# Kernel tuning notes

Measured on AMD Instinct MI355X. Metric: run time of the kernel, lower is better.

## Reference

```python
import jax, jax.numpy as jnp
import numpy as np

# Static config (matches init_kwargs / spatial layout)
SHAPES = ((64, 64), (32, 32), (16, 16))   # (H, W) per level, bev=256 at /4,/8,/16
B, HEADS, LEVELS, POINTS, C = 2, 8, 3, 4, 256
HD = C // HEADS
NV = sum(h * w for h, w in SHAPES)        # 5376
NQ = NV
TP = HEADS * LEVELS * POINTS              # 96


def setup_inputs() -> dict:
    key = jax.random.key(0)
    ks = jax.random.split(key, 10)
    s = 1.0 / np.sqrt(C)
    inp = {
        'query': jax.random.normal(ks[0], (B, NQ, C), dtype=jnp.float32),
        'reference_points': jax.random.uniform(ks[1], (B, NQ, 2), dtype=jnp.float32),
        'value': jax.random.normal(ks[2], (B, NV, C), dtype=jnp.float32),
        'Wv': jax.random.normal(ks[3], (C, C), dtype=jnp.float32) * s,
        'bv': jnp.zeros((C,), dtype=jnp.float32),
        # offset proj: small scale so sampling stays local-ish (orig init is 0)
        'Woff': jax.random.normal(ks[4], (TP * 2, C), dtype=jnp.float32) * (0.02 * s),
        'boff': jnp.zeros((TP * 2,), dtype=jnp.float32),
        'Wa': jax.random.normal(ks[5], (TP, C), dtype=jnp.float32) * s,
        'ba': jnp.zeros((TP,), dtype=jnp.float32),
        'Wo': jax.random.normal(ks[6], (C, C), dtype=jnp.float32) * s,
        'bo': jnp.zeros((C,), dtype=jnp.float32),
    }
    return inp


def _msda(query, reference_points, value, Wv, bv, Woff, boff, Wa, ba, Wo, bo):
    Bb, nq, _ = query.shape
    # value projection -> per-head values
    v = (value @ Wv.T + bv).reshape(Bb, NV, HEADS, HD)
    # sampling offsets: (B, NQ, HEADS, LEVELS, POINTS, 2)
    off = (query @ Woff.T + boff).reshape(Bb, nq, HEADS, LEVELS, POINTS, 2)
    # attention weights: softmax over LEVELS*POINTS jointly
    a = (query @ Wa.T + ba).reshape(Bb, nq, HEADS, LEVELS * POINTS)
    a = jax.nn.softmax(a, axis=-1).reshape(Bb, nq, HEADS, LEVELS, POINTS)
    # sampling locations in [0,1] (clamp matches torch .clamp(0,1))
    loc = jnp.clip(reference_points[:, :, None, None, None, :] + off, 0.0, 1.0)

    out = jnp.zeros((Bb, HEADS, nq, HD), dtype=query.dtype)
    start = 0
    for lvl, (H, W) in enumerate(SHAPES):
        n = H * W
        # (B, HEADS, H*W, HD) flattened level feature map per head
        vl = jnp.transpose(v[:, start:start + n].reshape(Bb, H, W, HEADS, HD),
                           (0, 3, 1, 2, 4)).reshape(Bb, HEADS, n, HD)
        loc_l = loc[:, :, :, lvl]                     # (B, NQ, HEADS, K, 2)
        # align_corners=False unnormalization: ((g+1)*size - 1)/2 with g=2*loc-1
        x = loc_l[..., 0] * W - 0.5
        y = loc_l[..., 1] * H - 0.5
        x0 = jnp.floor(x)
        y0 = jnp.floor(y)
        wx1 = x - x0
        wy1 = y - y0
        x0i = x0.astype(jnp.int32)
        y0i = y0.astype(jnp.int32)
        acc = jnp.zeros((Bb, HEADS, nq * POINTS, HD), dtype=query.dtype)
        for dy in (0, 1):
            for dx in (0, 1):
                ix = x0i + dx
                iy = y0i + dy
                wgt = (wx1 if dx else 1.0 - wx1) * (wy1 if dy else 1.0 - wy1)
                # zero padding outside the map (padding_mode='zeros')
                valid = (ix >= 0) & (ix < W) & (iy >= 0) & (iy < H)
                idx = jnp.clip(iy, 0, H - 1) * W + jnp.clip(ix, 0, W - 1)
                idx_t = jnp.transpose(idx, (0, 2, 1, 3)).reshape(Bb, HEADS, nq * POINTS)
                g = jnp.take_along_axis(vl, idx_t[..., None], axis=2)  # (B,H,NQ*K,HD)
                w_t = jnp.transpose(wgt * valid.astype(wgt.dtype),
                                    (0, 2, 1, 3)).reshape(Bb, HEADS, nq * POINTS, 1)
                acc = acc + g * w_t
        aw = jnp.transpose(a[:, :, :, lvl], (0, 2, 1, 3)).reshape(Bb, HEADS, nq * POINTS, 1)
        out = out + (acc * aw).reshape(Bb, HEADS, nq, POINTS, HD).sum(axis=3)
        start += n
    out = jnp.transpose(out, (0, 2, 1, 3)).reshape(Bb, nq, C)
    return out @ Wo.T + bo


def reference(query, reference_points, value, Wv, bv, Woff, boff, Wa, ba, Wo, bo):
    return _msda(query, reference_points, value, Wv, bv, Woff, boff, Wa, ba, Wo, bo)
```

## Files before the change

kernel.cpp:

```cpp
#include <hip/hip_runtime.h>
#include <hip/hip_bf16.h>
#include <cmath>

#define BATCH   2
#define NQ      5376
#define NV      5376
#define CDIM    256
#define HEADS   8
#define HD      32
#define LEVELS  3
#define POINTS  4
#define TP      96
#define MROWS   (BATCH*NQ)
#define NOFF    (TP*2)
#define NQA     (NOFF+TP)
#define NQAP    320

typedef __attribute__((ext_vector_type(8))) short bf16x8;
typedef __attribute__((ext_vector_type(4))) float f32x4;
typedef unsigned short u16;
typedef unsigned int   u32;

#define AS1 __attribute__((address_space(1)))
#define AS3 __attribute__((address_space(3)))

__device__ __forceinline__ void g2lds16(const void* g, void* l) {
    __builtin_amdgcn_global_load_lds((const AS1 void*)g, (AS3 void*)l, 16, 0, 0);
}

__device__ __forceinline__ u16 bf_of(float f) {
    union { __hip_bfloat16 h; u16 s; } u;
    u.h = __float2bfloat16(f);
    return u.s;
}
__device__ __forceinline__ float bf_back(u16 s) {
    return __uint_as_float((u32)s << 16);
}

__device__ __forceinline__ ushort4 cvt_hi(float4 v) {
    ushort4 h;
    h.x = bf_of(v.x); h.y = bf_of(v.y); h.z = bf_of(v.z); h.w = bf_of(v.w);
    return h;
}
__device__ __forceinline__ ushort4 cvt_lo(float4 v, ushort4 h) {
    ushort4 l;
    l.x = bf_of(v.x - bf_back(h.x));
    l.y = bf_of(v.y - bf_back(h.y));
    l.z = bf_of(v.z - bf_back(h.z));
    l.w = bf_of(v.w - bf_back(h.w));
    return l;
}

#define NVAL8  344064
#define NQRY8  344064
#define NWV8   8192
#define NWOFF8 6144
#define NWA8   3072
#define NWO8   8192
#define NPAD8  1024
#define PREP_BLOCKS 2792
__global__ __launch_bounds__(256) void prep_kernel(
    const float* __restrict__ value, const float* __restrict__ query,
    const float* __restrict__ Wv, const float* __restrict__ Woff,
    const float* __restrict__ Wa, const float* __restrict__ Wo,
    u16* __restrict__ val_hi, u16* __restrict__ val_lo,
    u16* __restrict__ q_hi, u16* __restrict__ wv_h,
    u16* __restrict__ wqa_h, u16* __restrict__ wo_h)
{
    int r = blockIdx.x * 256 + threadIdx.x;

    if (r < NVAL8) {
        const float4 a0 = *reinterpret_cast<const float4*>(value + (size_t)r * 8);
        const float4 a1 = *reinterpret_cast<const float4*>(value + (size_t)r * 8 + 4);
        const ushort4 h0 = cvt_hi(a0), h1 = cvt_hi(a1);
        *reinterpret_cast<ushort4*>(val_hi + (size_t)r * 8)     = h0;
        *reinterpret_cast<ushort4*>(val_hi + (size_t)r * 8 + 4) = h1;
        *reinterpret_cast<ushort4*>(val_lo + (size_t)r * 8)     = cvt_lo(a0, h0);
        *reinterpret_cast<ushort4*>(val_lo + (size_t)r * 8 + 4) = cvt_lo(a1, h1);
        return;
    }
    r -= NVAL8;
    if (r < NQRY8) {
        const float4 a0 = *reinterpret_cast<const float4*>(query + (size_t)r * 8);
        const float4 a1 = *reinterpret_cast<const float4*>(query + (size_t)r * 8 + 4);
        *reinterpret_cast<ushort4*>(q_hi + (size_t)r * 8)     = cvt_hi(a0);
        *reinterpret_cast<ushort4*>(q_hi + (size_t)r * 8 + 4) = cvt_hi(a1);
        return;
    }
    r -= NQRY8;
    if (r < NWV8) {
        const float4 a0 = *reinterpret_cast<const float4*>(Wv + (size_t)r * 8);
        const float4 a1 = *reinterpret_cast<const float4*>(Wv + (size_t)r * 8 + 4);
        *reinterpret_cast<ushort4*>(wv_h + (size_t)r * 8)     = cvt_hi(a0);
        *reinterpret_cast<ushort4*>(wv_h + (size_t)r * 8 + 4) = cvt_hi(a1);
        return;
    }
    r -= NWV8;
    if (r < NWOFF8) {
        const float4 a0 = *reinterpret_cast<const float4*>(Woff + (size_t)r * 8);
        const float4 a1 = *reinterpret_cast<const float4*>(Woff + (size_t)r * 8 + 4);
        *reinterpret_cast<ushort4*>(wqa_h + (size_t)r * 8)     = cvt_hi(a0);
        *reinterpret_cast<ushort4*>(wqa_h + (size_t)r * 8 + 4) = cvt_hi(a1);
        return;
    }
    r -= NWOFF8;
    if (r < NWA8) {
        const float4 a0 = *reinterpret_cast<const float4*>(Wa + (size_t)r * 8);
        const float4 a1 = *reinterpret_cast<const float4*>(Wa + (size_t)r * 8 + 4);
        u16* dst = wqa_h + (size_t)NOFF * CDIM;
        *reinterpret_cast<ushort4*>(dst + (size_t)r * 8)     = cvt_hi(a0);
        *reinterpret_cast<ushort4*>(dst + (size_t)r * 8 + 4) = cvt_hi(a1);
        return;
    }
    r -= NWA8;
    if (r < NWO8) {
        const float4 a0 = *reinterpret_cast<const float4*>(Wo + (size_t)r * 8);
        const float4 a1 = *reinterpret_cast<const float4*>(Wo + (size_t)r * 8 + 4);
        *reinterpret_cast<ushort4*>(wo_h + (size_t)r * 8)     = cvt_hi(a0);
        *reinterpret_cast<ushort4*>(wo_h + (size_t)r * 8 + 4) = cvt_hi(a1);
        return;
    }
    r -= NWO8;
    const ushort4 z = {0, 0, 0, 0};
    u16* dst = wqa_h + (size_t)NQA * CDIM;
    *reinterpret_cast<ushort4*>(dst + (size_t)r * 8)     = z;
    *reinterpret_cast<ushort4*>(dst + (size_t)r * 8 + 4) = z;
}

#define GBM 64
#define GBN 64
#define GBK 32

#define VBLOCKS (168 * 4)
#define K1_BLOCKS (VBLOCKS + 168 * 5)
#define K1_CPX (K1_BLOCKS / 8)

__global__ __launch_bounds__(256) void gemm_vqa_kernel(
    const u16* __restrict__ val_hi, const u16* __restrict__ val_lo,
    const u16* __restrict__ q_hi,
    const u16* __restrict__ wv_h, const u16* __restrict__ wqa_h,
    const float* __restrict__ bv, const float* __restrict__ boff,
    const float* __restrict__ ba,
    u16* __restrict__ vOut, u16* __restrict__ offOut, u16* __restrict__ aOut)
{
    __shared__ __align__(16) u16 sAh[2][GBM * GBK];
    __shared__ __align__(16) u16 sAl[2][GBM * GBK];
    __shared__ __align__(16) u16 sBh[2][GBM * GBK];

    const int bid0 = blockIdx.x;
    const int bid = (bid0 & 7) * K1_CPX + (bid0 >> 3);

    const bool vpath = bid < VBLOCKS;
    int m0, n0;
    if (vpath) { m0 = (bid >> 2) * GBM;          n0 = (bid & 3) * GBM; }
    else       { const int b2 = bid - VBLOCKS;
                 m0 = (b2 / 5) * GBM;            n0 = (b2 % 5) * GBM; }

    const int tid  = threadIdx.x;
    const int lane = tid & 63;
    const int wave = tid >> 6;
    const int wr   = wave & 1;
    const int wc   = wave >> 1;
    const int qm   = lane & 15;
    const int quad = lane >> 4;

    const int arow = (wave << 4) + (lane >> 2);
    const int ak   = (lane & 3) * 8;

    const u16* Asrc_h = (vpath ? val_hi : q_hi) + (size_t)(m0 + arow) * CDIM + ak;
    const u16* Asrc_l = val_lo + (size_t)(m0 + arow) * CDIM + ak;
    const u16* Bsrc   = (vpath ? wv_h : wqa_h) + (size_t)(n0 + arow) * CDIM + ak;

    f32x4 acc[2][2];
    #pragma unroll
    for (int i = 0; i < 2; ++i)
        #pragma unroll
        for (int j = 0; j < 2; ++j)
            acc[i][j] = (f32x4){0.f, 0.f, 0.f, 0.f};

    {
        g2lds16(Asrc_h, &sAh[0][wave * 512]);
        if (vpath) g2lds16(Asrc_l, &sAl[0][wave * 512]);
        g2lds16(Bsrc, &sBh[0][wave * 512]);
    }
    __syncthreads();

    int cur = 0;
    for (int k0 = 0; k0 < CDIM; k0 += GBK) {
        if (k0 + GBK < CDIM) {
            g2lds16(Asrc_h + k0 + GBK, &sAh[cur ^ 1][wave * 512]);
            if (vpath) g2lds16(Asrc_l + k0 + GBK, &sAl[cur ^ 1][wave * 512]);
            g2lds16(Bsrc + k0 + GBK, &sBh[cur ^ 1][wave * 512]);
        }

        bf16x8 fah[2], fal[2], fbh[2];
        #pragma unroll
        for (int x = 0; x < 2; ++x) {
            const int rm = wr * 32 + x * 16 + qm;
            const int rn = wc * 32 + x * 16 + qm;
            fah[x] = *reinterpret_cast<const bf16x8*>(&sAh[cur][rm * GBK + quad * 8]);
            fbh[x] = *reinterpret_cast<const bf16x8*>(&sBh[cur][rn * GBK + quad * 8]);
            if (vpath)
                fal[x] = *reinterpret_cast<const bf16x8*>(&sAl[cur][rm * GBK + quad * 8]);
        }
        #pragma unroll
        for (int mi = 0; mi < 2; ++mi)
            #pragma unroll
            for (int ni = 0; ni < 2; ++ni) {
                acc[mi][ni] = __builtin_amdgcn_mfma_f32_16x16x32_bf16(
                    fah[mi], fbh[ni], acc[mi][ni], 0, 0, 0);
                if (vpath)
                    acc[mi][ni] = __builtin_amdgcn_mfma_f32_16x16x32_bf16(
                        fal[mi], fbh[ni], acc[mi][ni], 0, 0, 0);
            }
        __syncthreads();
        cur ^= 1;
    }

    #pragma unroll
    for (int mi = 0; mi < 2; ++mi) {
        #pragma unroll
        for (int ni = 0; ni < 2; ++ni) {
            const int n = n0 + wc * 32 + ni * 16 + qm;
            if (vpath) {
                const float bn = bv[n];
                #pragma unroll
                for (int r = 0; r < 4; ++r) {
                    const int m = m0 + wr * 32 + mi * 16 + quad * 4 + r;
                    const float val = acc[mi][ni][r] + bn;
                    const int b = m / NV, rr = m - b * NV;
                    const int h = n >> 5, c = n & 31;
                    vOut[(((size_t)b * HEADS + h) * NV + rr) * HD + c] = bf_of(val);
                }
            } else {
                if (n >= NQA) continue;
                const float bn = (n < NOFF) ? boff[n] : ba[n - NOFF];
                #pragma unroll
                for (int r = 0; r < 4; ++r) {
                    const int m = m0 + wr * 32 + mi * 16 + quad * 4 + r;
                    const float val = acc[mi][ni][r] + bn;
                    if (n < NOFF)
                        offOut[(size_t)m * NOFF + n] = bf_of(val);
                    else
                        aOut[(size_t)m * TP + (n - NOFF)] = bf_of(val);
                }
            }
        }
    }
}

#define K3_BLOCKS ((MROWS / GBM) * 4)
#define K3_CPX (K3_BLOCKS / 8)

__global__ __launch_bounds__(256) void gemm_out_kernel(
    const u16* __restrict__ Ah, const u16* __restrict__ wo_h,
    const float* __restrict__ bias, float* __restrict__ Cout)
{
    __shared__ __align__(16) u16 sAh[2][GBM * GBK];
    __shared__ __align__(16) u16 sBh[2][GBM * GBK];

    const int bid0 = blockIdx.x;
    const int bid = (bid0 & 7) * K3_CPX + (bid0 >> 3);
    const int m0 = (bid >> 2) * GBM;
    const int n0 = (bid & 3) * GBM;

    const int tid  = threadIdx.x;
    const int lane = tid & 63;
    const int wave = tid >> 6;
    const int wr   = wave & 1;
    const int wc   = wave >> 1;
    const int qm   = lane & 15;
    const int quad = lane >> 4;

    const int arow = (wave << 4) + (lane >> 2);
    const int ak   = (lane & 3) * 8;

    const u16* Asrc = Ah   + (size_t)(m0 + arow) * CDIM + ak;
    const u16* Bsrc = wo_h + (size_t)(n0 + arow) * CDIM + ak;

    f32x4 acc[2][2];
    #pragma unroll
    for (int i = 0; i < 2; ++i)
        #pragma unroll
        for (int j = 0; j < 2; ++j)
            acc[i][j] = (f32x4){0.f, 0.f, 0.f, 0.f};

    g2lds16(Asrc, &sAh[0][wave * 512]);
    g2lds16(Bsrc, &sBh[0][wave * 512]);
    __syncthreads();

    int cur = 0;
    for (int k0 = 0; k0 < CDIM; k0 += GBK) {
        if (k0 + GBK < CDIM) {
            g2lds16(Asrc + k0 + GBK, &sAh[cur ^ 1][wave * 512]);
            g2lds16(Bsrc + k0 + GBK, &sBh[cur ^ 1][wave * 512]);
        }

        bf16x8 fah[2], fbh[2];
        #pragma unroll
        for (int x = 0; x < 2; ++x) {
            const int rm = wr * 32 + x * 16 + qm;
            const int rn = wc * 32 + x * 16 + qm;
            fah[x] = *reinterpret_cast<const bf16x8*>(&sAh[cur][rm * GBK + quad * 8]);
            fbh[x] = *reinterpret_cast<const bf16x8*>(&sBh[cur][rn * GBK + quad * 8]);
        }
        #pragma unroll
        for (int mi = 0; mi < 2; ++mi)
            #pragma unroll
            for (int ni = 0; ni < 2; ++ni)
                acc[mi][ni] = __builtin_amdgcn_mfma_f32_16x16x32_bf16(
                    fah[mi], fbh[ni], acc[mi][ni], 0, 0, 0);
        __syncthreads();
        cur ^= 1;
    }

    #pragma unroll
    for (int mi = 0; mi < 2; ++mi) {
        #pragma unroll
        for (int ni = 0; ni < 2; ++ni) {
            const int n = n0 + wc * 32 + ni * 16 + qm;
            const float bn = bias[n];
            #pragma unroll
            for (int r = 0; r < 4; ++r) {
                const int m = m0 + wr * 32 + mi * 16 + quad * 4 + r;
                Cout[(size_t)m * CDIM + n] = acc[mi][ni][r] + bn;
            }
        }
    }
}

__global__ __launch_bounds__(256) void msda_core_kernel(
    const u16* __restrict__ off,
    const u16* __restrict__ alog,
    const float* __restrict__ refp,
    const u16*   __restrict__ v,
    u16* __restrict__ t_hi)
{
    const int tid = threadIdx.x;
    const int bq0 = blockIdx.x * 4;

    __shared__ float s_w[4][TP];
    __shared__ int   s_idx[4][TP][4];
    __shared__ float s_twt[4][TP][4];

    #pragma unroll
    for (int base = 0; base < 4 * TP; base += 256) {
        const int idx = base + tid;
        if (idx < 4 * TP) {
            const int q = idx / TP, j = idx - q * TP;
            s_w[q][j] = bf_back(alog[(size_t)(bq0 + q) * TP + j]);
        }
    }
    __syncthreads();

    if (tid < 32) {
        const int q = tid >> 3, h = tid & 7;
        float mx = -1e30f;
        #pragma unroll
        for (int i = 0; i < 12; ++i) mx = fmaxf(mx, s_w[q][h * 12 + i]);
        float e[12];
        float sum = 0.f;
        #pragma unroll
        for (int i = 0; i < 12; ++i) {
            e[i] = expf(s_w[q][h * 12 + i] - mx);
            sum += e[i];
        }
        const float inv = 1.f / sum;
        #pragma unroll
        for (int i = 0; i < 12; ++i) s_w[q][h * 12 + i] = e[i] * inv;
    }
    __syncthreads();

    #pragma unroll
    for (int base = 0; base < 4 * TP; base += 256) {
        const int idx = base + tid;
        if (idx < 4 * TP) {
            const int q = idx / TP, j = idx - q * TP;
            const int bq = bq0 + q;
            const int jj = j % 12;
            const int l  = jj >> 2;
            const int Wl    = (l == 0) ? 64 : (l == 1) ? 32 : 16;
            const int start = (l == 0) ? 0 : (l == 1) ? 4096 : 5120;

            const float refx = refp[(size_t)bq * 2 + 0];
            const float refy = refp[(size_t)bq * 2 + 1];
            const float ox = bf_back(off[(size_t)bq * NOFF + j * 2 + 0]);
            const float oy = bf_back(off[(size_t)bq * NOFF + j * 2 + 1]);
            const float lx = fminf(fmaxf(refx + ox, 0.f), 1.f) * (float)Wl - 0.5f;
            const float ly = fminf(fmaxf(refy + oy, 0.f), 1.f) * (float)Wl - 0.5f;
            const float fx0 = floorf(lx), fy0 = floorf(ly);
            const int   x0  = (int)fx0,   y0  = (int)fy0;
            const float wx1 = lx - fx0,   wy1 = ly - fy0;
            const float wx0 = 1.f - wx1,  wy0 = 1.f - wy1;
            const float aw  = s_w[q][j];

            #pragma unroll
            for (int k = 0; k < 4; ++k) {
                const int dx = k & 1, dy = k >> 1;
                const int xi = x0 + dx, yi = y0 + dy;
                const bool ok = (xi >= 0) & (xi < Wl) & (yi >= 0) & (yi < Wl);
                const int xc = min(max(xi, 0), Wl - 1);
                const int yc = min(max(yi, 0), Wl - 1);
                s_idx[q][j][k] = (start + yc * Wl + xc) * (HD * 2);
                const float wxy = (dx ? wx1 : wx0) * (dy ? wy1 : wy0);
                s_twt[q][j][k] = ok ? aw * wxy : 0.f;
            }
        }
    }
    __syncthreads();

    const int qsel = tid >> 6;
    const int ht   = tid & 63;
    const int h    = ht >> 3;
    const int sub  = ht & 7;
    const int oct  = sub & 3;
    const int rep  = sub >> 2;
    const int bq   = bq0 + qsel;
    const int b    = bq / NQ;
    const char* vb = (const char*)v + (((size_t)b * HEADS + h) * NV) * (HD * 2) + oct * 16;

    float acc[8] = {};
    #pragma unroll
    for (int g = 0; g < 3; ++g) {
        uint4 raw[8];
        float wt[8];
        #pragma unroll
        for (int pp = 0; pp < 2; ++pp) {
            const int j = h * 12 + rep * 6 + g * 2 + pp;
            const int4   ix = *reinterpret_cast<const int4*>(&s_idx[qsel][j][0]);
            const float4 tw = *reinterpret_cast<const float4*>(&s_twt[qsel][j][0]);
            raw[pp * 4 + 0] = *reinterpret_cast<const uint4*>(vb + ix.x);
            raw[pp * 4 + 1] = *reinterpret_cast<const uint4*>(vb + ix.y);
            raw[pp * 4 + 2] = *reinterpret_cast<const uint4*>(vb + ix.z);
            raw[pp * 4 + 3] = *reinterpret_cast<const uint4*>(vb + ix.w);
            wt[pp * 4 + 0] = tw.x; wt[pp * 4 + 1] = tw.y;
            wt[pp * 4 + 2] = tw.z; wt[pp * 4 + 3] = tw.w;
        }
        #pragma unroll
        for (int k = 0; k < 8; ++k) {
            acc[0] += wt[k] * __uint_as_float(raw[k].x << 16);
            acc[1] += wt[k] * __uint_as_float(raw[k].x & 0xffff0000u);
            acc[2] += wt[k] * __uint_as_float(raw[k].y << 16);
            acc[3] += wt[k] * __uint_as_float(raw[k].y & 0xffff0000u);
            acc[4] += wt[k] * __uint_as_float(raw[k].z << 16);
            acc[5] += wt[k] * __uint_as_float(raw[k].z & 0xffff0000u);
            acc[6] += wt[k] * __uint_as_float(raw[k].w << 16);
            acc[7] += wt[k] * __uint_as_float(raw[k].w & 0xffff0000u);
        }
    }

    #pragma unroll
    for (int c = 0; c < 8; ++c)
        acc[c] += __shfl_xor(acc[c], 4);

    if (rep == 0) {
        uint4 o;
        o.x = (u32)bf_of(acc[0]) | ((u32)bf_of(acc[1]) << 16);
        o.y = (u32)bf_of(acc[2]) | ((u32)bf_of(acc[3]) << 16);
        o.z = (u32)bf_of(acc[4]) | ((u32)bf_of(acc[5]) << 16);
        o.w = (u32)bf_of(acc[6]) | ((u32)bf_of(acc[7]) << 16);
        const size_t base = (size_t)bq * CDIM + h * HD + oct * 8;
        *reinterpret_cast<uint4*>(t_hi + base) = o;
    }
}

extern "C" void kernel_launch(void* const* d_in, const int* in_sizes, int n_in,
                              void* d_out, int out_size, void* d_ws, size_t ws_size,
                              hipStream_t stream)
{
    const float* query = (const float*)d_in[0];
    const float* refp  = (const float*)d_in[1];
    const float* value = (const float*)d_in[2];
    const float* Wv    = (const float*)d_in[3];
    const float* bv    = (const float*)d_in[4];
    const float* Woff  = (const float*)d_in[5];
    const float* boff  = (const float*)d_in[6];
    const float* Wa    = (const float*)d_in[7];
    const float* ba    = (const float*)d_in[8];
    const float* Wo    = (const float*)d_in[9];
    const float* bo    = (const float*)d_in[10];
    float* out = (float*)d_out;

    char* w = (char*)d_ws;
    const size_t SZ_T = (size_t)MROWS * CDIM * 2;
    u16* v_bf16 = (u16*)(w);
    u16* t_hi   = (u16*)(w + 1 * SZ_T);
    u16* ws_off = (u16*)(w + 2 * SZ_T);
    u16* ws_a   = (u16*)(w + 2 * SZ_T + (size_t)MROWS * NOFF * 2);
    char* w2    = w + 2 * SZ_T + (size_t)MROWS * NQA * 2;
    u16* val_hi = (u16*)(w2);
    u16* val_lo = (u16*)(w2 + 1 * SZ_T);
    u16* q_hi   = (u16*)(w2 + 2 * SZ_T);
    u16* wv_h   = (u16*)(w2 + 3 * SZ_T);
    u16* wqa_h  = (u16*)(w2 + 3 * SZ_T + (size_t)CDIM * CDIM * 2);
    u16* wo_h   = (u16*)(w2 + 3 * SZ_T + (size_t)CDIM * CDIM * 2
                              + (size_t)NQAP * CDIM * 2);

    const dim3 blk(256);

    prep_kernel<<<dim3(PREP_BLOCKS), blk, 0, stream>>>(
        value, query, Wv, Woff, Wa, Wo,
        val_hi, val_lo, q_hi, wv_h, wqa_h, wo_h);

    gemm_vqa_kernel<<<dim3(K1_BLOCKS), blk, 0, stream>>>(
        val_hi, val_lo, q_hi, wv_h, wqa_h,
        bv, boff, ba, v_bf16, ws_off, ws_a);

    msda_core_kernel<<<dim3(MROWS / 4), blk, 0, stream>>>(
        ws_off, ws_a, refp, v_bf16, t_hi);

    gemm_out_kernel<<<dim3(K3_BLOCKS), blk, 0, stream>>>(
        t_hi, wo_h, bo, out);
}
```

Before: 134.4 us.

## Fuse four kernels into one persistent kernel with grid barriers

Merges the prep, QKV-style projection GEMM, deformable sampling and output GEMM kernels into a single persistent kernel. Each phase uses grid-stride loops, and phases are separated by atomic-counter grid barriers. The aim is to remove three kernel launch gaps and tail effects between stages. In exchange it adds a memset, spin-wait barriers and a fixed grid of up to 1024 blocks. Correctness depends on all blocks being co-resident, and each phase loses per-kernel tuning such as the block swizzle in the GEMM.

```diff
diff --git a/kernel.cpp b/kernel.cpp
--- a/kernel.cpp
+++ b/kernel.cpp
@@ -51,6 +51,19 @@
     return l;
 }
 
+__device__ __forceinline__ void grid_barrier(unsigned* bar, int nb) {
+    __syncthreads();
+    if (threadIdx.x == 0) {
+        __builtin_amdgcn_fence(__ATOMIC_RELEASE, "agent");
+        atomicAdd(bar, 1u);
+        while (__hip_atomic_load(bar, __ATOMIC_RELAXED,
+                                 __HIP_MEMORY_SCOPE_AGENT) < (unsigned)nb)
+            __builtin_amdgcn_s_sleep(2);
+        __builtin_amdgcn_fence(__ATOMIC_ACQUIRE, "agent");
+    }
+    __syncthreads();
+}
+
 #define NVAL8  344064
 #define NQRY8  344064
 #define NWV8   8192
@@ -58,8 +71,10 @@
 #define NWA8   3072
 #define NWO8   8192
 #define NPAD8  1024
-#define PREP_BLOCKS 2792
-__global__ __launch_bounds__(256) void prep_kernel(
+#define PREP_ITEMS (NVAL8+NQRY8+NWV8+NWOFF8+NWA8+NWO8+NPAD8)
+#define PREP_BLOCKS (PREP_ITEMS/256)
+
+__device__ __forceinline__ void prep_item(int r,
     const float* __restrict__ value, const float* __restrict__ query,
     const float* __restrict__ Wv, const float* __restrict__ Woff,
     const float* __restrict__ Wa, const float* __restrict__ Wo,
@@ -67,8 +82,6 @@
     u16* __restrict__ q_hi, u16* __restrict__ wv_h,
     u16* __restrict__ wqa_h, u16* __restrict__ wo_h)
 {
-    int r = blockIdx.x * 256 + threadIdx.x;
-
     if (r < NVAL8) {
         const float4 a0 = *reinterpret_cast<const float4*>(value + (size_t)r * 8);
         const float4 a1 = *reinterpret_cast<const float4*>(value + (size_t)r * 8 + 4);
@@ -77,65 +90,74 @@
         *reinterpret_cast<ushort4*>(val_hi + (size_t)r * 8 + 4) = h1;
         *reinterpret_cast<ushort4*>(val_lo + (size_t)r * 8)     = cvt_lo(a0, h0);
         *reinterpret_cast<ushort4*>(val_lo + (size_t)r * 8 + 4) = cvt_lo(a1, h1);
-        return;
+    } else {
+        r -= NVAL8;
+        if (r < NQRY8) {
+            const float4 a0 = *reinterpret_cast<const float4*>(query + (size_t)r * 8);
+            const float4 a1 = *reinterpret_cast<const float4*>(query + (size_t)r * 8 + 4);
+            *reinterpret_cast<ushort4*>(q_hi + (size_t)r * 8)     = cvt_hi(a0);
+            *reinterpret_cast<ushort4*>(q_hi + (size_t)r * 8 + 4) = cvt_hi(a1);
+        } else {
+            r -= NQRY8;
+            if (r < NWV8) {
+                const float4 a0 = *reinterpret_cast<const float4*>(Wv + (size_t)r * 8);
+                const float4 a1 = *reinterpret_cast<const float4*>(Wv + (size_t)r * 8 + 4);
+                *reinterpret_cast<ushort4*>(wv_h + (size_t)r * 8)     = cvt_hi(a0);
+                *reinterpret_cast<ushort4*>(wv_h + (size_t)r * 8 + 4) = cvt_hi(a1);
+            } else {
+                r -= NWV8;
+                if (r < NWOFF8) {
+                    const float4 a0 = *reinterpret_cast<const float4*>(Woff + (size_t)r * 8);
+                    const float4 a1 = *reinterpret_cast<const float4*>(Woff + (size_t)r * 8 + 4);
+                    *reinterpret_cast<ushort4*>(wqa_h + (size_t)r * 8)     = cvt_hi(a0);
+                    *reinterpret_cast<ushort4*>(wqa_h + (size_t)r * 8 + 4) = cvt_hi(a1);
+                } else {
+                    r -= NWOFF8;
+                    if (r < NWA8) {
+                        const float4 a0 = *reinterpret_cast<const float4*>(Wa + (size_t)r * 8);
+                        const float4 a1 = *reinterpret_cast<const float4*>(Wa + (size_t)r * 8 + 4);
+                        u16* dst = wqa_h + (size_t)NOFF * CDIM;
+                        *reinterpret_cast<ushort4*>(dst + (size_t)r * 8)     = cvt_hi(a0);
+                        *reinterpret_cast<ushort4*>(dst + (size_t)r * 8 + 4) = cvt_hi(a1);
+                    } else {
+                        r -= NWA8;
+                        if (r < NWO8) {
+                            const float4 a0 = *reinterpret_cast<const float4*>(Wo + (size_t)r * 8);
+                            const float4 a1 = *reinterpret_cast<const float4*>(Wo + (size_t)r * 8 + 4);
+                            *reinterpret_cast<ushort4*>(wo_h + (size_t)r * 8)     = cvt_hi(a0);
+                            *reinterpret_cast<ushort4*>(wo_h + (size_t)r * 8 + 4) = cvt_hi(a1);
+                        } else {
+                            r -= NWO8;
+                            const ushort4 z = {0, 0, 0, 0};
+                            u16* dst = wqa_h + (size_t)NQA * CDIM;
+                            *reinterpret_cast<ushort4*>(dst + (size_t)r * 8)     = z;
+                            *reinterpret_cast<ushort4*>(dst + (size_t)r * 8 + 4) = z;
+                        }
+                    }
+                }
+            }
+        }
     }
-    r -= NVAL8;
-    if (r < NQRY8) {
-        const float4 a0 = *reinterpret_cast<const float4*>(query + (size_t)r * 8);
-        const float4 a1 = *reinterpret_cast<const float4*>(query + (size_t)r * 8 + 4);
-        *reinterpret_cast<ushort4*>(q_hi + (size_t)r * 8)     = cvt_hi(a0);
-        *reinterpret_cast<ushort4*>(q_hi + (size_t)r * 8 + 4) = cvt_hi(a1);
-        return;
-    }
-    r -= NQRY8;
-    if (r < NWV8) {
-        const float4 a0 = *reinterpret_cast<const float4*>(Wv + (size_t)r * 8);
-        const float4 a1 = *reinterpret_cast<const float4*>(Wv + (size_t)r * 8 + 4);
-        *reinterpret_cast<ushort4*>(wv_h + (size_t)r * 8)     = cvt_hi(a0);
-        *reinterpret_cast<ushort4*>(wv_h + (size_t)r * 8 + 4) = cvt_hi(a1);
-        return;
-    }
-    r -= NWV8;
-    if (r < NWOFF8) {
-        const float4 a0 = *reinterpret_cast<const float4*>(Woff + (size_t)r * 8);
-        const float4 a1 = *reinterpret_cast<const float4*>(Woff + (size_t)r * 8 + 4);
-        *reinterpret_cast<ushort4*>(wqa_h + (size_t)r * 8)     = cvt_hi(a0);
-        *reinterpret_cast<ushort4*>(wqa_h + (size_t)r * 8 + 4) = cvt_hi(a1);
-        return;
-    }
-    r -= NWOFF8;
-    if (r < NWA8) {
-        const float4 a0 = *reinterpret_cast<const float4*>(Wa + (size_t)r * 8);
-        const float4 a1 = *reinterpret_cast<const float4*>(Wa + (size_t)r * 8 + 4);
-        u16* dst = wqa_h + (size_t)NOFF * CDIM;
-        *reinterpret_cast<ushort4*>(dst + (size_t)r * 8)     = cvt_hi(a0);
-        *reinterpret_cast<ushort4*>(dst + (size_t)r * 8 + 4) = cvt_hi(a1);
-        return;
-    }
-    r -= NWA8;
-    if (r < NWO8) {
-        const float4 a0 = *reinterpret_cast<const float4*>(Wo + (size_t)r * 8);
-        const float4 a1 = *reinterpret_cast<const float4*>(Wo + (size_t)r * 8 + 4);
-        *reinterpret_cast<ushort4*>(wo_h + (size_t)r * 8)     = cvt_hi(a0);
-        *reinterpret_cast<ushort4*>(wo_h + (size_t)r * 8 + 4) = cvt_hi(a1);
-        return;
-    }
-    r -= NWO8;
-    const ushort4 z = {0, 0, 0, 0};
-    u16* dst = wqa_h + (size_t)NQA * CDIM;
-    *reinterpret_cast<ushort4*>(dst + (size_t)r * 8)     = z;
-    *reinterpret_cast<ushort4*>(dst + (size_t)r * 8 + 4) = z;
+}
+
+__device__ __forceinline__ void phase_prep(int bid, int nb,
+    const float* value, const float* query, const float* Wv,
+    const float* Woff, const float* Wa, const float* Wo,
+    u16* val_hi, u16* val_lo, u16* q_hi,
+    u16* wv_h, u16* wqa_h, u16* wo_h)
+{
+    for (int r = bid * 256 + (int)threadIdx.x; r < PREP_ITEMS; r += nb * 256)
+        prep_item(r, value, query, Wv, Woff, Wa, Wo,
+                  val_hi, val_lo, q_hi, wv_h, wqa_h, wo_h);
 }
 
 #define GBM 64
 #define GBN 64
 #define GBK 32
-
 #define VBLOCKS (168 * 4)
 #define K1_BLOCKS (VBLOCKS + 168 * 5)
-#define K1_CPX (K1_BLOCKS / 8)
-
-__global__ __launch_bounds__(256) void gemm_vqa_kernel(
+
+__device__ __forceinline__ void phase_vqa(char* smem, int bid, int nb,
     const u16* __restrict__ val_hi, const u16* __restrict__ val_lo,
     const u16* __restrict__ q_hi,
     const u16* __restrict__ wv_h, const u16* __restrict__ wqa_h,
@@ -143,18 +165,9 @@
     const float* __restrict__ ba,
     u16* __restrict__ vOut, u16* __restrict__ offOut, u16* __restrict__ aOut)
 {
-    __shared__ __align__(16) u16 sAh[2][GBM * GBK];
-    __shared__ __align__(16) u16 sAl[2][GBM * GBK];
-    __shared__ __align__(16) u16 sBh[2][GBM * GBK];
-
-    const int bid0 = blockIdx.x;
-    const int bid = (bid0 & 7) * K1_CPX + (bid0 >> 3);
-
-    const bool vpath = bid < VBLOCKS;
-    int m0, n0;
-    if (vpath) { m0 = (bid >> 2) * GBM;          n0 = (bid & 3) * GBM; }
-    else       { const int b2 = bid - VBLOCKS;
-                 m0 = (b2 / 5) * GBM;            n0 = (b2 % 5) * GBM; }
+    u16 (*sAh)[GBM * GBK] = reinterpret_cast<u16(*)[GBM * GBK]>(smem);
+    u16 (*sAl)[GBM * GBK] = reinterpret_cast<u16(*)[GBM * GBK]>(smem + 8192);
+    u16 (*sBh)[GBM * GBK] = reinterpret_cast<u16(*)[GBM * GBK]>(smem + 16384);
 
     const int tid  = threadIdx.x;
     const int lane = tid & 63;
@@ -163,106 +176,243 @@
     const int wc   = wave >> 1;
     const int qm   = lane & 15;
     const int quad = lane >> 4;
-
     const int arow = (wave << 4) + (lane >> 2);
     const int ak   = (lane & 3) * 8;
 
-    const u16* Asrc_h = (vpath ? val_hi : q_hi) + (size_t)(m0 + arow) * CDIM + ak;
-    const u16* Asrc_l = val_lo + (size_t)(m0 + arow) * CDIM + ak;
-    const u16* Bsrc   = (vpath ? wv_h : wqa_h) + (size_t)(n0 + arow) * CDIM + ak;
-
-    f32x4 acc[2][2];
-    #pragma unroll
-    for (int i = 0; i < 2; ++i)
-        #pragma unroll
-        for (int j = 0; j < 2; ++j)
-            acc[i][j] = (f32x4){0.f, 0.f, 0.f, 0.f};
-
-    {
+    for (int t = bid; t < K1_BLOCKS; t += nb) {
+        const bool vpath = t < VBLOCKS;
+        int m0, n0;
+        if (vpath) { m0 = (t >> 2) * GBM;           n0 = (t & 3) * GBM; }
+        else       { const int b2 = t - VBLOCKS;
+                     m0 = (b2 / 5) * GBM;           n0 = (b2 % 5) * GBM; }
+
+        const u16* Asrc_h = (vpath ? val_hi : q_hi) + (size_t)(m0 + arow) * CDIM + ak;
+        const u16* Asrc_l = val_lo + (size_t)(m0 + arow) * CDIM + ak;
+        const u16* Bsrc   = (vpath ? wv_h : wqa_h) + (size_t)(n0 + arow) * CDIM + ak;
+
+        f32x4 acc[2][2];
+        #pragma unroll
+        for (int i = 0; i < 2; ++i)
+            #pragma unroll
+            for (int j = 0; j < 2; ++j)
+                acc[i][j] = (f32x4){0.f, 0.f, 0.f, 0.f};
+
         g2lds16(Asrc_h, &sAh[0][wave * 512]);
         if (vpath) g2lds16(Asrc_l, &sAl[0][wave * 512]);
         g2lds16(Bsrc, &sBh[0][wave * 512]);
+        __syncthreads();
+
+        int cur = 0;
+        for (int k0 = 0; k0 < CDIM; k0 += GBK) {
+            if (k0 + GBK < CDIM) {
+                g2lds16(Asrc_h + k0 + GBK, &sAh[cur ^ 1][wave * 512]);
+                if (vpath) g2lds16(Asrc_l + k0 + GBK, &sAl[cur ^ 1][wave * 512]);
+                g2lds16(Bsrc + k0 + GBK, &sBh[cur ^ 1][wave * 512]);
+            }
+
+            bf16x8 fah[2], fal[2], fbh[2];
+            #pragma unroll
+            for (int x = 0; x < 2; ++x) {
+                const int rm = wr * 32 + x * 16 + qm;
+                const int rn = wc * 32 + x * 16 + qm;
+                fah[x] = *reinterpret_cast<const bf16x8*>(&sAh[cur][rm * GBK + quad * 8]);
+                fbh[x] = *reinterpret_cast<const bf16x8*>(&sBh[cur][rn * GBK + quad * 8]);
+                if (vpath)
+                    fal[x] = *reinterpret_cast<const bf16x8*>(&sAl[cur][rm * GBK + quad * 8]);
+            }
+            #pragma unroll
+            for (int mi = 0; mi < 2; ++mi)
+                #pragma unroll
+                for (int ni = 0; ni < 2; ++ni) {
+                    acc[mi][ni] = __builtin_amdgcn_mfma_f32_16x16x32_bf16(
+                        fah[mi], fbh[ni], acc[mi][ni], 0, 0, 0);
+                    if (vpath)
+                        acc[mi][ni] = __builtin_amdgcn_mfma_f32_16x16x32_bf16(
+                            fal[mi], fbh[ni], acc[mi][ni], 0, 0, 0);
+                }
+            __syncthreads();
+            cur ^= 1;
+        }
+
+        #pragma unroll
+        for (int mi = 0; mi < 2; ++mi) {
+            #pragma unroll
+            for (int ni = 0; ni < 2; ++ni) {
+                const int n = n0 + wc * 32 + ni * 16 + qm;
+                if (vpath) {
+                    const float bn = bv[n];
+                    #pragma unroll
+                    for (int r = 0; r < 4; ++r) {
+                        const int m = m0 + wr * 32 + mi * 16 + quad * 4 + r;
+                        const float val = acc[mi][ni][r] + bn;
+                        const int b = m / NV, rr = m - b * NV;
+                        const int h = n >> 5, c = n & 31;
+                        vOut[(((size_t)b * HEADS + h) * NV + rr) * HD + c] = bf_of(val);
+                    }
+                } else {
+                    if (n < NQA) {
+                        const float bn = (n < NOFF) ? boff[n] : ba[n - NOFF];
+                        #pragma unroll
+                        for (int r = 0; r < 4; ++r) {
+                            const int m = m0 + wr * 32 + mi * 16 + quad * 4 + r;
+                            const float val = acc[mi][ni][r] + bn;
+                            if (n < NOFF)
+                                offOut[(size_t)m * NOFF + n] = bf_of(val);
+                            else
+                                aOut[(size_t)m * TP + (n - NOFF)] = bf_of(val);
+                        }
+                    }
+                }
+            }
+        }
     }
-    __syncthreads();
-
-    int cur = 0;
-    for (int k0 = 0; k0 < CDIM; k0 += GBK) {
-        if (k0 + GBK < CDIM) {
-            g2lds16(Asrc_h + k0 + GBK, &sAh[cur ^ 1][wave * 512]);
-            if (vpath) g2lds16(Asrc_l + k0 + GBK, &sAl[cur ^ 1][wave * 512]);
-            g2lds16(Bsrc + k0 + GBK, &sBh[cur ^ 1][wave * 512]);
-        }
-
-        bf16x8 fah[2], fal[2], fbh[2];
-        #pragma unroll
-        for (int x = 0; x < 2; ++x) {
-            const int rm = wr * 32 + x * 16 + qm;
-            const int rn = wc * 32 + x * 16 + qm;
-            fah[x] = *reinterpret_cast<const bf16x8*>(&sAh[cur][rm * GBK + quad * 8]);
-            fbh[x] = *reinterpret_cast<const bf16x8*>(&sBh[cur][rn * GBK + quad * 8]);
-            if (vpath)
-                fal[x] = *reinterpret_cast<const bf16x8*>(&sAl[cur][rm * GBK + quad * 8]);
-        }
-        #pragma unroll
-        for (int mi = 0; mi < 2; ++mi)
-            #pragma unroll
-            for (int ni = 0; ni < 2; ++ni) {
-                acc[mi][ni] = __builtin_amdgcn_mfma_f32_16x16x32_bf16(
-                    fah[mi], fbh[ni], acc[mi][ni], 0, 0, 0);
-                if (vpath)
-                    acc[mi][ni] = __builtin_amdgcn_mfma_f32_16x16x32_bf16(
-                        fal[mi], fbh[ni], acc[mi][ni], 0, 0, 0);
-            }
+}
+
+__device__ __forceinline__ void phase_msda(char* smem, int bid, int nb,
+    const u16* __restrict__ off, const u16* __restrict__ alog,
+    const float* __restrict__ refp, const u16* __restrict__ v,
+    u16* __restrict__ t_hi)
+{
+    float (*s_w)[TP]      = reinterpret_cast<float(*)[TP]>(smem);
+    int   (*s_idx)[TP][4] = reinterpret_cast<int(*)[TP][4]>(smem + 1536);
+    float (*s_twt)[TP][4] = reinterpret_cast<float(*)[TP][4]>(smem + 7680);
+
+    const int tid = threadIdx.x;
+
+    for (int g0 = bid; g0 < MROWS / 4; g0 += nb) {
         __syncthreads();
-        cur ^= 1;
+        const int bq0 = g0 * 4;
+
+        #pragma unroll
+        for (int base = 0; base < 4 * TP; base += 256) {
+            const int idx = base + tid;
+            if (idx < 4 * TP) {
+                const int q = idx / TP, j = idx - q * TP;
+                s_w[q][j] = bf_back(alog[(size_t)(bq0 + q) * TP + j]);
+            }
+        }
+        __syncthreads();
+
+        if (tid < 32) {
+            const int q = tid >> 3, h = tid & 7;
+            float mx = -1e30f;
+            #pragma unroll
+            for (int i = 0; i < 12; ++i) mx = fmaxf(mx, s_w[q][h * 12 + i]);
+            float e[12];
+            float sum = 0.f;
+            #pragma unroll
+            for (int i = 0; i < 12; ++i) {
+                e[i] = expf(s_w[q][h * 12 + i] - mx);
+                sum += e[i];
+            }
+            const float inv = 1.f / sum;
+            #pragma unroll
+            for (int i = 0; i < 12; ++i) s_w[q][h * 12 + i] = e[i] * inv;
+        }
+        __syncthreads();
+
+        #pragma unroll
+        for (int base = 0; base < 4 * TP; base += 256) {
+            const int idx = base + tid;
+            if (idx < 4 * TP) {
+                const int q = idx / TP, j = idx - q * TP;
+                const int bq = bq0 + q;
+                const int jj = j % 12;
+                const int l  = jj >> 2;
+                const int Wl    = (l == 0) ? 64 : (l == 1) ? 32 : 16;
+                const int start = (l == 0) ? 0 : (l == 1) ? 4096 : 5120;
+
+                const float refx = refp[(size_t)bq * 2 + 0];
+                const float refy = refp[(size_t)bq * 2 + 1];
+                const float ox = bf_back(off[(size_t)bq * NOFF + j * 2 + 0]);
+                const float oy = bf_back(off[(size_t)bq * NOFF + j * 2 + 1]);
+                const float lx = fminf(fmaxf(refx + ox, 0.f), 1.f) * (float)Wl - 0.5f;
+                const float ly = fminf(fmaxf(refy + oy, 0.f), 1.f) * (float)Wl - 0.5f;
+                const float fx0 = floorf(lx), fy0 = floorf(ly);
+                const int   x0  = (int)fx0,   y0  = (int)fy0;
+                const float wx1 = lx - fx0,   wy1 = ly - fy0;
+                const float wx0 = 1.f - wx1,  wy0 = 1.f - wy1;
+                const float aw  = s_w[q][j];
+
+                #pragma unroll
+                for (int k = 0; k < 4; ++k) {
+                    const int dx = k & 1, dy = k >> 1;
+                    const int xi = x0 + dx, yi = y0 + dy;
+                    const bool ok = (xi >= 0) & (xi < Wl) & (yi >= 0) & (yi < Wl);
+                    const int xc = min(max(xi, 0), Wl - 1);
+                    const int yc = min(max(yi, 0), Wl - 1);
+                    s_idx[q][j][k] = (start + yc * Wl + xc) * (HD * 2);
+                    const float wxy = (dx ? wx1 : wx0) * (dy ? wy1 : wy0);
+                    s_twt[q][j][k] = ok ? aw * wxy : 0.f;
+                }
+            }
+        }
+        __syncthreads();
+
+        const int qsel = tid >> 6;
+        const int ht   = tid & 63;
+        const int h    = ht >> 3;
+        const int sub  = ht & 7;
+        const int oct  = sub & 3;
+        const int rep  = sub >> 2;
+        const int bq   = bq0 + qsel;
+        const int b    = bq / NQ;
+        const char* vb = (const char*)v + (((size_t)b * HEADS + h) * NV) * (HD * 2) + oct * 16;
+
+        float acc[8] = {};
+        #pragma unroll
+        for (int g = 0; g < 3; ++g) {
+            uint4 raw[8];
+            float wt[8];
+            #pragma unroll
+            for (int pp = 0; pp < 2; ++pp) {
+                const int j = h * 12 + rep * 6 + g * 2 + pp;
+                const int4   ix = *reinterpret_cast<const int4*>(&s_idx[qsel][j][0]);
+                const float4 tw = *reinterpret_cast<const float4*>(&s_twt[qsel][j][0]);
+                raw[pp * 4 + 0] = *reinterpret_cast<const uint4*>(vb + ix.x);
+                raw[pp * 4 + 1] = *reinterpret_cast<const uint4*>(vb + ix.y);
+                raw[pp * 4 + 2] = *reinterpret_cast<const uint4*>(vb + ix.z);
+                raw[pp * 4 + 3] = *reinterpret_cast<const uint4*>(vb + ix.w);
+                wt[pp * 4 + 0] = tw.x; wt[pp * 4 + 1] = tw.y;
+                wt[pp * 4 + 2] = tw.z; wt[pp * 4 + 3] = tw.w;
+            }
+            #pragma unroll
+            for (int k = 0; k < 8; ++k) {
+                acc[0] += wt[k] * __uint_as_float(raw[k].x << 16);
+                acc[1] += wt[k] * __uint_as_float(raw[k].x & 0xffff0000u);
+                acc[2] += wt[k] * __uint_as_float(raw[k].y << 16);
+                acc[3] += wt[k] * __uint_as_float(raw[k].y & 0xffff0000u);
+                acc[4] += wt[k] * __uint_as_float(raw[k].z << 16);
+                acc[5] += wt[k] * __uint_as_float(raw[k].z & 0xffff0000u);
+                acc[6] += wt[k] * __uint_as_float(raw[k].w << 16);
+                acc[7] += wt[k] * __uint_as_float(raw[k].w & 0xffff0000u);
+            }
+        }
+
+        #pragma unroll
+        for (int c = 0; c < 8; ++c)
+            acc[c] += __shfl_xor(acc[c], 4);
+
+        if (rep == 0) {
+            uint4 o;
+            o.x = (u32)bf_of(acc[0]) | ((u32)bf_of(acc[1]) << 16);
+            o.y = (u32)bf_of(acc[2]) | ((u32)bf_of(acc[3]) << 16);
+            o.z = (u32)bf_of(acc[4]) | ((u32)bf_of(acc[5]) << 16);
+            o.w = (u32)bf_of(acc[6]) | ((u32)bf_of(acc[7]) << 16);
+            const size_t base = (size_t)bq * CDIM + h * HD + oct * 8;
+            *reinterpret_cast<uint4*>(t_hi + base) = o;
+        }
     }
-
-    #pragma unroll
-    for (int mi = 0; mi < 2; ++mi) {
-        #pragma unroll
-        for (int ni = 0; ni < 2; ++ni) {
-            const int n = n0 + wc * 32 + ni * 16 + qm;
-            if (vpath) {
-                const float bn = bv[n];
-                #pragma unroll
-                for (int r = 0; r < 4; ++r) {
-                    const int m = m0 + wr * 32 + mi * 16 + quad * 4 + r;
-                    const float val = acc[mi][ni][r] + bn;
-                    const int b = m / NV, rr = m - b * NV;
-                    const int h = n >> 5, c = n & 31;
-                    vOut[(((size_t)b * HEADS + h) * NV + rr) * HD + c] = bf_of(val);
-                }
-            } else {
-                if (n >= NQA) continue;
-                const float bn = (n < NOFF) ? boff[n] : ba[n - NOFF];
-                #pragma unroll
-                for (int r = 0; r < 4; ++r) {
-                    const int m = m0 + wr * 32 + mi * 16 + quad * 4 + r;
-                    const float val = acc[mi][ni][r] + bn;
-                    if (n < NOFF)
-                        offOut[(size_t)m * NOFF + n] = bf_of(val);
-                    else
-                        aOut[(size_t)m * TP + (n - NOFF)] = bf_of(val);
-                }
-            }
-        }
-    }
 }
 
 #define K3_BLOCKS ((MROWS / GBM) * 4)
-#define K3_CPX (K3_BLOCKS / 8)
-
-__global__ __launch_bounds__(256) void gemm_out_kernel(
+
+__device__ __forceinline__ void phase_out(char* smem, int bid, int nb,
     const u16* __restrict__ Ah, const u16* __restrict__ wo_h,
     const float* __restrict__ bias, float* __restrict__ Cout)
 {
-    __shared__ __align__(16) u16 sAh[2][GBM * GBK];
-    __shared__ __align__(16) u16 sBh[2][GBM * GBK];
-
-    const int bid0 = blockIdx.x;
-    const int bid = (bid0 & 7) * K3_CPX + (bid0 >> 3);
-    const int m0 = (bid >> 2) * GBM;
-    const int n0 = (bid & 3) * GBM;
+    u16 (*sAh)[GBM * GBK] = reinterpret_cast<u16(*)[GBM * GBK]>(smem);
+    u16 (*sBh)[GBM * GBK] = reinterpret_cast<u16(*)[GBM * GBK]>(smem + 8192);
 
     const int tid  = threadIdx.x;
     const int lane = tid & 63;
@@ -271,197 +421,130 @@
     const int wc   = wave >> 1;
     const int qm   = lane & 15;
     const int quad = lane >> 4;
-
     const int arow = (wave << 4) + (lane >> 2);
     const int ak   = (lane & 3) * 8;
 
-    const u16* Asrc = Ah   + (size_t)(m0 + arow) * CDIM + ak;
-    const u16* Bsrc = wo_h + (size_t)(n0 + arow) * CDIM + ak;
-
-    f32x4 acc[2][2];
-    #pragma unroll
-    for (int i = 0; i < 2; ++i)
-        #pragma unroll
-        for (int j = 0; j < 2; ++j)
-            acc[i][j] = (f32x4){0.f, 0.f, 0.f, 0.f};
-
-    g2lds16(Asrc, &sAh[0][wave * 512]);
-    g2lds16(Bsrc, &sBh[0][wave * 512]);
-    __syncthreads();
-
-    int cur = 0;
-    for (int k0 = 0; k0 < CDIM; k0 += GBK) {
-        if (k0 + GBK < CDIM) {
-            g2lds16(Asrc + k0 + GBK, &sAh[cur ^ 1][wave * 512]);
-            g2lds16(Bsrc + k0 + GBK, &sBh[cur ^ 1][wave * 512]);
-        }
-
-        bf16x8 fah[2], fbh[2];
-        #pragma unroll
-        for (int x = 0; x < 2; ++x) {
-            const int rm = wr * 32 + x * 16 + qm;
-            const int rn = wc * 32 + x * 16 + qm;
-            fah[x] = *reinterpret_cast<const bf16x8*>(&sAh[cur][rm * GBK + quad * 8]);
-            fbh[x] = *reinterpret_cast<const bf16x8*>(&sBh[cur][rn * GBK + quad * 8]);
-        }
-        #pragma unroll
-        for (int mi = 0; mi < 2; ++mi)
-            #pragma unroll
-            for (int ni = 0; ni < 2; ++ni)
-                acc[mi][ni] = __builtin_amdgcn_mfma_f32_16x16x32_bf16(
-                    fah[mi], fbh[ni], acc[mi][ni], 0, 0, 0);
+    for (int t = bid; t < K3_BLOCKS; t += nb) {
+        const int m0 = (t >> 2) * GBM;
+        const int n0 = (t & 3) * GBN;
+
+        const u16* Asrc = Ah   + (size_t)(m0 + arow) * CDIM + ak;
+        const u16* Bsrc = wo_h + (size_t)(n0 + arow) * CDIM + ak;
+
+        f32x4 acc[2][2];
+        #pragma unroll
+        for (int i = 0; i < 2; ++i)
+            #pragma unroll
+            for (int j = 0; j < 2; ++j)
+                acc[i][j] = (f32x4){0.f, 0.f, 0.f, 0.f};
+
+        g2lds16(Asrc, &sAh[0][wave * 512]);
+        g2lds16(Bsrc, &sBh[0][wave * 512]);
         __syncthreads();
-        cur ^= 1;
+
+        int cur = 0;
+        for (int k0 = 0; k0 < CDIM; k0 += GBK) {
+            if (k0 + GBK < CDIM) {
+                g2lds16(Asrc + k0 + GBK, &sAh[cur ^ 1][wave * 512]);
+                g2lds16(Bsrc + k0 + GBK, &sBh[cur ^ 1][wave * 512]);
+            }
+
+            bf16x8 fah[2], fbh[2];
+            #pragma unroll
+            for (int x = 0; x < 2; ++x) {
+                const int rm = wr * 32 + x * 16 + qm;
+                const int rn = wc * 32 + x * 16 + qm;
+                fah[x] = *reinterpret_cast<const bf16x8*>(&sAh[cur][rm * GBK + quad * 8]);
+                fbh[x] = *reinterpret_cast<const bf16x8*>(&sBh[cur][rn * GBK + quad * 8]);
+            }
+            #pragma unroll
+            for (int mi = 0; mi < 2; ++mi)
+                #pragma unroll
+                for (int ni = 0; ni < 2; ++ni)
+                    acc[mi][ni] = __builtin_amdgcn_mfma_f32_16x16x32_bf16(
+                        fah[mi], fbh[ni], acc[mi][ni], 0, 0, 0);
+            __syncthreads();
+            cur ^= 1;
+        }
+
+        #pragma unroll
+        for (int mi = 0; mi < 2; ++mi) {
+            #pragma unroll
+            for (int ni = 0; ni < 2; ++ni) {
+                const int n = n0 + wc * 32 + ni * 16 + qm;
+                const float bn = bias[n];
+                #pragma unroll
+                for (int r = 0; r < 4; ++r) {
+                    const int m = m0 + wr * 32 + mi * 16 + quad * 4 + r;
+                    Cout[(size_t)m * CDIM + n] = acc[mi][ni][r] + bn;
+                }
+            }
+        }
     }
-
-    #pragma unroll
-    for (int mi = 0; mi < 2; ++mi) {
-        #pragma unroll
-        for (int ni = 0; ni < 2; ++ni) {
-            const int n = n0 + wc * 32 + ni * 16 + qm;
-            const float bn = bias[n];
-            #pragma unroll
-            for (int r = 0; r < 4; ++r) {
-                const int m = m0 + wr * 32 + mi * 16 + quad * 4 + r;
-                Cout[(size_t)m * CDIM + n] = acc[mi][ni][r] + bn;
-            }
-        }
-    }
-}
-
-__global__ __launch_bounds__(256) void msda_core_kernel(
-    const u16* __restrict__ off,
-    const u16* __restrict__ alog,
+}
+
+__global__ __launch_bounds__(256, 4) void fused_all(
+    const float* __restrict__ value, const float* __restrict__ query,
+    const float* __restrict__ Wv, const float* __restrict__ Woff,
+    const float* __restrict__ Wa, const float* __restrict__ Wo,
+    const float* __restrict__ bv, const float* __restrict__ boff,
+    const float* __restrict__ ba, const float* __restrict__ bo,
     const float* __restrict__ refp,
-    const u16*   __restrict__ v,
-    u16* __restrict__ t_hi)
-{
-    const int tid = threadIdx.x;
-    const int bq0 = blockIdx.x * 4;
-
-    __shared__ float s_w[4][TP];
-    __shared__ int   s_idx[4][TP][4];
-    __shared__ float s_twt[4][TP][4];
-
-    #pragma unroll
-    for (int base = 0; base < 4 * TP; base += 256) {
-        const int idx = base + tid;
-        if (idx < 4 * TP) {
-            const int q = idx / TP, j = idx - q * TP;
-            s_w[q][j] = bf_back(alog[(size_t)(bq0 + q) * TP + j]);
-        }
-    }
-    __syncthreads();
-
-    if (tid < 32) {
-        const int q = tid >> 3, h = tid & 7;
-        float mx = -1e30f;
-        #pragma unroll
-        for (int i = 0; i < 12; ++i) mx = fmaxf(mx, s_w[q][h * 12 + i]);
-        float e[12];
-        float sum = 0.f;
-        #pragma unroll
-        for (int i = 0; i < 12; ++i) {
-            e[i] = expf(s_w[q][h * 12 + i] - mx);
-            sum += e[i];
-        }
-        const float inv = 1.f / sum;
-        #pragma unroll
-        for (int i = 0; i < 12; ++i) s_w[q][h * 12 + i] = e[i] * inv;
-    }
-    __syncthreads();
-
-    #pragma unroll
-    for (int base = 0; base < 4 * TP; base += 256) {
-        const int idx = base + tid;
-        if (idx < 4 * TP) {
-            const int q = idx / TP, j = idx - q * TP;
-            const int bq = bq0 + q;
-            const int jj = j % 12;
-            const int l  = jj >> 2;
-            const int Wl    = (l == 0) ? 64 : (l == 1) ? 32 : 16;
-            const int start = (l == 0) ? 0 : (l == 1) ? 4096 : 5120;
-
-            const float refx = refp[(size_t)bq * 2 + 0];
-            const float refy = refp[(size_t)bq * 2 + 1];
-            const float ox = bf_back(off[(size_t)bq * NOFF + j * 2 + 0]);
-            const float oy = bf_back(off[(size_t)bq * NOFF + j * 2 + 1]);
-            const float lx = fminf(fmaxf(refx + ox, 0.f), 1.f) * (float)Wl - 0.5f;
-            const float ly = fminf(fmaxf(refy + oy, 0.f), 1.f) * (float)Wl - 0.5f;
-            const float fx0 = floorf(lx), fy0 = floorf(ly);
-            const int   x0  = (int)fx0,   y0  = (int)fy0;
-            const float wx1 = lx - fx0,   wy1 = ly - fy0;
-            const float wx0 = 1.f - wx1,  wy0 = 1.f - wy1;
-            const float aw  = s_w[q][j];
-
-            #pragma unroll
-            for (int k = 0; k < 4; ++k) {
-                const int dx = k & 1, dy = k >> 1;
-                const int xi = x0 + dx, yi = y0 + dy;
-                const bool ok = (xi >= 0) & (xi < Wl) & (yi >= 0) & (yi < Wl);
-                const int xc = min(max(xi, 0), Wl - 1);
-                const int yc = min(max(yi, 0), Wl - 1);
-                s_idx[q][j][k] = (start + yc * Wl + xc) * (HD * 2);
-                const float wxy = (dx ? wx1 : wx0) * (dy ? wy1 : wy0);
-                s_twt[q][j][k] = ok ? aw * wxy : 0.f;
-            }
-        }
-    }
-    __syncthreads();
-
-    const int qsel = tid >> 6;
-    const int ht   = tid & 63;
-    const int h    = ht >> 3;
-    const int sub  = ht & 7;
-    const int oct  = sub & 3;
-    const int rep  = sub >> 2;
-    const int bq   = bq0 + qsel;
-    const int b    = bq / NQ;
-    const char* vb = (const char*)v + (((size_t)b * HEADS + h) * NV) * (HD * 2) + oct * 16;
-
-    float acc[8] = {};
-    #pragma unroll
-    for (int g = 0; g < 3; ++g) {
-        uint4 raw[8];
-        float wt[8];
-        #pragma unroll
-        for (int pp = 0; pp < 2; ++pp) {
-            const int j = h * 12 + rep * 6 + g * 2 + pp;
-            const int4   ix = *reinterpret_cast<const int4*>(&s_idx[qsel][j][0]);
-            const float4 tw = *reinterpret_cast<const float4*>(&s_twt[qsel][j][0]);
-            raw[pp * 4 + 0] = *reinterpret_cast<const uint4*>(vb + ix.x);
-            raw[pp * 4 + 1] = *reinterpret_cast<const uint4*>(vb + ix.y);
-            raw[pp * 4 + 2] = *reinterpret_cast<const uint4*>(vb + ix.z);
-            raw[pp * 4 + 3] = *reinterpret_cast<const uint4*>(vb + ix.w);
-            wt[pp * 4 + 0] = tw.x; wt[pp * 4 + 1] = tw.y;
-            wt[pp * 4 + 2] = tw.z; wt[pp * 4 + 3] = tw.w;
-        }
-        #pragma unroll
-        for (int k = 0; k < 8; ++k) {
-            acc[0] += wt[k] * __uint_as_float(raw[k].x << 16);
-            acc[1] += wt[k] * __uint_as_float(raw[k].x & 0xffff0000u);
-            acc[2] += wt[k] * __uint_as_float(raw[k].y << 16);
-            acc[3] += wt[k] * __uint_as_float(raw[k].y & 0xffff0000u);
-            acc[4] += wt[k] * __uint_as_float(raw[k].z << 16);
-            acc[5] += wt[k] * __uint_as_float(raw[k].z & 0xffff0000u);
-            acc[6] += wt[k] * __uint_as_float(raw[k].w << 16);
-            acc[7] += wt[k] * __uint_as_float(raw[k].w & 0xffff0000u);
-        }
-    }
-
-    #pragma unroll
-    for (int c = 0; c < 8; ++c)
-        acc[c] += __shfl_xor(acc[c], 4);
-
-    if (rep == 0) {
-        uint4 o;
-        o.x = (u32)bf_of(acc[0]) | ((u32)bf_of(acc[1]) << 16);
-        o.y = (u32)bf_of(acc[2]) | ((u32)bf_of(acc[3]) << 16);
-        o.z = (u32)bf_of(acc[4]) | ((u32)bf_of(acc[5]) << 16);
-        o.w = (u32)bf_of(acc[6]) | ((u32)bf_of(acc[7]) << 16);
-        const size_t base = (size_t)bq * CDIM + h * HD + oct * 8;
-        *reinterpret_cast<uint4*>(t_hi + base) = o;
-    }
+    u16* val_hi, u16* val_lo, u16* q_hi,
+    u16* wv_h, u16* wqa_h, u16* wo_h,
+    u16* v_bf16, u16* ws_off, u16* ws_a, u16* t_hi,
+    float* out, unsigned* bars)
+{
+    __shared__ __align__(16) char smem[24576];
+    const int bid = blockIdx.x;
+    const int nb  = gridDim.x;
+
+    phase_prep(bid, nb, value, query, Wv, Woff, Wa, Wo,
+               val_hi, val_lo, q_hi, wv_h, wqa_h, wo_h);
+    grid_barrier(bars + 0, nb);
+
+    phase_vqa(smem, bid, nb, val_hi, val_lo, q_hi, wv_h, wqa_h,
+              bv, boff, ba, v_bf16, ws_off, ws_a);
+    grid_barrier(bars + 32, nb);
+
+    phase_msda(smem, bid, nb, ws_off, ws_a, refp, v_bf16, t_hi);
+    grid_barrier(bars + 64, nb);
+
+    phase_out(smem, bid, nb, t_hi, wo_h, bo, out);
+}
+
+__global__ __launch_bounds__(256) void prep_k(
+    const float* value, const float* query, const float* Wv,
+    const float* Woff, const float* Wa, const float* Wo,
+    u16* val_hi, u16* val_lo, u16* q_hi, u16* wv_h, u16* wqa_h, u16* wo_h)
+{
+    phase_prep(blockIdx.x, gridDim.x, value, query, Wv, Woff, Wa, Wo,
+               val_hi, val_lo, q_hi, wv_h, wqa_h, wo_h);
+}
+
+__global__ __launch_bounds__(256) void vqa_k(
+    const u16* val_hi, const u16* val_lo, const u16* q_hi,
+    const u16* wv_h, const u16* wqa_h,
+    const float* bv, const float* boff, const float* ba,
+    u16* vOut, u16* offOut, u16* aOut)
+{
+    __shared__ __align__(16) char smem[24576];
+    phase_vqa(smem, blockIdx.x, gridDim.x, val_hi, val_lo, q_hi, wv_h, wqa_h,
+              bv, boff, ba, vOut, offOut, aOut);
+}
+
+__global__ __launch_bounds__(256) void msda_k(
+    const u16* off, const u16* alog, const float* refp, const u16* v, u16* t_hi)
+{
+    __shared__ __align__(16) char smem[13824];
+    phase_msda(smem, blockIdx.x, gridDim.x, off, alog, refp, v, t_hi);
+}
+
+__global__ __launch_bounds__(256) void out_k(
+    const u16* Ah, const u16* wo_h, const float* bias, float* Cout)
+{
+    __shared__ __align__(16) char smem[16384];
+    phase_out(smem, blockIdx.x, gridDim.x, Ah, wo_h, bias, Cout);
 }
 
 extern "C" void kernel_launch(void* const* d_in, const int* in_sizes, int n_in,
@@ -495,20 +578,33 @@
     u16* wqa_h  = (u16*)(w2 + 3 * SZ_T + (size_t)CDIM * CDIM * 2);
     u16* wo_h   = (u16*)(w2 + 3 * SZ_T + (size_t)CDIM * CDIM * 2
                               + (size_t)NQAP * CDIM * 2);
+    unsigned* bars = (unsigned*)(w2 + 3 * SZ_T + (size_t)CDIM * CDIM * 2
+                              + (size_t)NQAP * CDIM * 2
+                              + (size_t)CDIM * CDIM * 2);
 
     const dim3 blk(256);
 
-    prep_kernel<<<dim3(PREP_BLOCKS), blk, 0, stream>>>(
-        value, query, Wv, Woff, Wa, Wo,
-        val_hi, val_lo, q_hi, wv_h, wqa_h, wo_h);
-
-    gemm_vqa_kernel<<<dim3(K1_BLOCKS), blk, 0, stream>>>(
-        val_hi, val_lo, q_hi, wv_h, wqa_h,
-        bv, boff, ba, v_bf16, ws_off, ws_a);
-
-    msda_core_kernel<<<dim3(MROWS / 4), blk, 0, stream>>>(
-        ws_off, ws_a, refp, v_bf16, t_hi);
-
-    gemm_out_kernel<<<dim3(K3_BLOCKS), blk, 0, stream>>>(
-        t_hi, wo_h, bo, out);
-}
+    int mb = 0;
+    hipError_t qe = hipOccupancyMaxActiveBlocksPerMultiprocessor(&mb, fused_all, 256, 0);
+
+    if (qe == hipSuccess && mb >= 1) {
+        int grid = mb * 256;
+        if (grid > 1024) grid = 1024;
+        hipMemsetAsync(bars, 0, 512, stream);
+        fused_all<<<dim3(grid), blk, 0, stream>>>(
+            value, query, Wv, Woff, Wa, Wo, bv, boff, ba, bo, refp,
+            val_hi, val_lo, q_hi, wv_h, wqa_h, wo_h,
+            v_bf16, ws_off, ws_a, t_hi, out, bars);
+    } else {
+        prep_k<<<dim3(PREP_BLOCKS), blk, 0, stream>>>(
+            value, query, Wv, Woff, Wa, Wo,
+            val_hi, val_lo, q_hi, wv_h, wqa_h, wo_h);
+        vqa_k<<<dim3(K1_BLOCKS), blk, 0, stream>>>(
+            val_hi, val_lo, q_hi, wv_h, wqa_h, bv, boff, ba,
+            v_bf16, ws_off, ws_a);
+        msda_k<<<dim3(MROWS / 4), blk, 0, stream>>>(
+            ws_off, ws_a, refp, v_bf16, t_hi);
+        out_k<<<dim3(K3_BLOCKS), blk, 0, stream>>>(
+            t_hi, wo_h, bo, out);
+    }
+}
```

After: 301.6 us. 2.24x slower.
